# Performance work log

Measured on AMD Instinct MI355X. Metric: run time of the kernel, lower is better.

The kernel has to match this reference:

```python
import jax, jax.numpy as jnp
import numpy as np

CONV_K = 4
C_EXP = 8.0  # Griffin exponent constant
EPS = 1.1920929e-07  # torch RMSNorm default eps = finfo(float32).eps


def rmsnorm(x, w):
    return x * jax.lax.rsqrt(jnp.mean(x * x, axis=-1, keepdims=True) + EPS) * w


def gelu(x):
    return jax.nn.gelu(x, approximate=False)  # torch F.gelu default (erf)


def setup_inputs() -> dict:
    B, T, D = 16, 1024, 1024
    H = 4 * D  # GatedMLP hidden
    key = jax.random.key(0)
    ks = jax.random.split(key, 16)
    s = 0.02
    return {
        "x_seq": jax.random.normal(ks[0], (B, T, D), jnp.float32),
        "h0": jnp.zeros((B, D), jnp.float32),
        "conv_buf": jax.random.normal(ks[1], (B, CONV_K - 1, D), jnp.float32),
        "norm1_w": jnp.ones((D,), jnp.float32),
        "W1": jax.random.normal(ks[2], (D, D), jnp.float32) * s,
        "conv_w": jax.random.normal(ks[3], (D, CONV_K), jnp.float32) * s,
        "conv_b": jnp.zeros((D,), jnp.float32),
        "Wa": jax.random.normal(ks[4], (D, D), jnp.float32) * s,
        "ba": jnp.zeros((D,), jnp.float32),
        "Wx": jax.random.normal(ks[5], (D, D), jnp.float32) * s,
        "bx": jnp.zeros((D,), jnp.float32),
        "log_lambda": jnp.linspace(0.0, 4.0, D).astype(jnp.float32),
        "W2": jax.random.normal(ks[6], (D, D), jnp.float32) * s,
        "Wout": jax.random.normal(ks[7], (D, D), jnp.float32) * s,
        "norm2_w": jnp.ones((D,), jnp.float32),
        "Wg": jax.random.normal(ks[8], (H, D), jnp.float32) * s,
        "Wu": jax.random.normal(ks[9], (H, D), jnp.float32) * s,
        "Wo": jax.random.normal(ks[10], (D, H), jnp.float32) * s,
    }


def _block(x_seq, h0, conv_buf, norm1_w, W1, conv_w, conv_b, Wa, ba, Wx, bx,
           log_lambda, W2, Wout, norm2_w, Wg, Wu, Wo):
    B, T, D = x_seq.shape
    normed = rmsnorm(x_seq, norm1_w)
    b1 = normed @ W1.T                                   # (B,T,D)
    padded = jnp.concatenate([conv_buf, b1], axis=1)     # (B,T+3,D)
    # depthwise causal conv (cross-correlation, matching torch Conv1d)
    b1_conv = conv_b
    for k in range(CONV_K):
        b1_conv = b1_conv + padded[:, k:k + T, :] * conv_w[:, k]
    new_conv_buf = padded[:, -(CONV_K - 1):, :]

    # RG-LRU: precompute gates, scan only the diagonal linear recurrence
    r = jax.nn.sigmoid(b1_conv @ Wa.T + ba)
    i = jax.nn.sigmoid(b1_conv @ Wx.T + bx)
    a = jnp.exp((C_EXP * r) * jax.nn.log_sigmoid(log_lambda))  # sigmoid(L)**(c*r)
    gate = jnp.sqrt(jnp.clip((1.0 - a) * (1.0 + a), 1e-06))
    u = gate * (i * b1_conv)

    def step(h, au):
        a_t, u_t = au
        h = a_t * h + u_t
        return h, h

    new_h, outs = jax.lax.scan(step, h0,
                               (jnp.swapaxes(a, 0, 1), jnp.swapaxes(u, 0, 1)))
    b1_out = jnp.swapaxes(outs, 0, 1)                    # (B,T,D)

    b2 = gelu(normed @ W2.T)
    recurrent_out = (b1_out * b2) @ Wout.T
    x1 = x_seq + recurrent_out

    n2 = rmsnorm(x1, norm2_w)
    mlp = (gelu(n2 @ Wg.T) * (n2 @ Wu.T)) @ Wo.T         # GeGLU gated MLP
    x2 = x1 + mlp
    return x2, new_h, new_conv_buf


def reference(x_seq, h0, conv_buf, norm1_w, W1, conv_w, conv_b, Wa, ba, Wx, bx,
              log_lambda, W2, Wout, norm2_w, Wg, Wu, Wo):
    return _block(x_seq, h0, conv_buf, norm1_w, W1, conv_w, conv_b, Wa, ba,
                  Wx, bx, log_lambda, W2, Wout, norm2_w, Wg, Wu, Wo)
```

## Files before the change

### kernel.cpp

```cpp
#include <hip/hip_runtime.h>
#include <hip/hip_bf16.h>
#include <cstdint>

using bf16 = __hip_bfloat16;
typedef __attribute__((ext_vector_type(8))) short bf16x8;
typedef __attribute__((ext_vector_type(4))) float f32x4;

#define NB 16
#define NT_ 1024
#define ND 1024
#define NH 4096
#define NM (NB * NT_)

enum { EPI_BF16 = 0, EPI_OM, EPI_U, EPI_GELU, EPI_GELU_MUL, EPI_X1, EPI_X2 };

__device__ __forceinline__ float sigm(float x) { return 1.0f / (1.0f + expf(-x)); }
__device__ __forceinline__ float gelu_f(float x) { return 0.5f * x * (1.0f + erff(x * 0.7071067811865476f)); }
__device__ __forceinline__ float b2f(bf16 h) { return __bfloat162float(h); }
__device__ __forceinline__ bf16  f2b(float x) { return __float2bfloat16(x); }

__device__ __forceinline__ void gl_lds16(const bf16* g, void* l) {
  __builtin_amdgcn_global_load_lds((const __attribute__((address_space(1))) void*)g,
                                   (__attribute__((address_space(3))) void*)l, 16, 0, 0);
}

template <int EPI>
__global__ __launch_bounds__(512, 2)
void gemm256(const bf16* __restrict__ A, const bf16* __restrict__ Bw,
             int M, int N, int K,
             const float* __restrict__ biasf, const float* __restrict__ vecf,
             const bf16* __restrict__ auxb, const bf16* __restrict__ auxb2,
             const float* __restrict__ auxf,
             float* __restrict__ outf, bf16* __restrict__ outb)
{
  (void)M;
  __shared__ __align__(16) bf16x8 lds8[8192];
  const int tid  = (int)threadIdx.x;
  const int wave = tid >> 6, lane = tid & 63;
  const int lr = lane & 15, lq = lane >> 4;
  const int wm = wave >> 2, wn = wave & 3;

  const int nwg = (int)gridDim.x;
  const int swz = ((int)blockIdx.x & 7) * (nwg >> 3) + ((int)blockIdx.x >> 3);
  const int nbx = N >> 8;
  const int by = swz / nbx, bx = swz - by * nbx;
  const int m0 = by << 8, n0 = bx << 8;
  const int NT = K >> 6;

  const bf16* __restrict__ Ag = A  + (long)m0 * K;
  const bf16* __restrict__ Bg = Bw + (long)n0 * K;

  const int lrow = lane >> 2;
  const int kbs  = (lane & 3) ^ (((lane >> 5) & 1) << 1);
  const int lqs = lq ^ ((lr & 8) >> 2);
  const int aRd = wm * 512 + lr * 4 + lqs;
  const int bRd = 2048 + wn * 256 + lr * 4 + lqs;

  const bf16 *gA0, *gA1, *gA2, *gA3, *gB0, *gB1, *gB2, *gB3;
  int dA0, dA1, dA2, dA3;
  {
    const int cc0 = wave * 2, cc1 = wave * 2 + 1;
    const int kh0 = cc0 >> 3, kh1 = cc1 >> 3;
    const int r00 = (cc0 & 7) << 4, r01 = (cc1 & 7) << 4;
    const int kc0 = kh0 * 32 + kbs * 8, kc1 = kh1 * 32 + kbs * 8;
    gA0 = Ag + (long)(r00 + lrow) * K + kc0;
    gA1 = Ag + (long)(r01 + lrow) * K + kc1;
    gA2 = Ag + (long)(128 + r00 + lrow) * K + kc0;
    gA3 = Ag + (long)(128 + r01 + lrow) * K + kc1;
    gB0 = Bg + (long)(r00 + lrow) * K + kc0;
    gB1 = Bg + (long)(r01 + lrow) * K + kc1;
    gB2 = Bg + (long)(128 + r00 + lrow) * K + kc0;
    gB3 = Bg + (long)(128 + r01 + lrow) * K + kc1;
    dA0 = kh0 * 16384 + (r00      ) * 64 + lane * 16;
    dA1 = kh1 * 16384 + (r01      ) * 64 + lane * 16;
    dA2 = kh0 * 16384 + (128 + r00) * 64 + lane * 16;
    dA3 = kh1 * 16384 + (128 + r01) * 64 + lane * 16;
  }

#define STAGE_ALL(BUFOFF) do { \
    char* Lb_ = ((char*)lds8) + (BUFOFF); \
    gl_lds16(gA0, Lb_ + dA0);          gl_lds16(gA1, Lb_ + dA1); \
    gl_lds16(gA2, Lb_ + dA2);          gl_lds16(gA3, Lb_ + dA3); \
    gl_lds16(gB0, Lb_ + 32768 + dA0);  gl_lds16(gB1, Lb_ + 32768 + dA1); \
    gl_lds16(gB2, Lb_ + 32768 + dA2);  gl_lds16(gB3, Lb_ + 32768 + dA3); \
    gA0 += 64; gA1 += 64; gA2 += 64; gA3 += 64; \
    gB0 += 64; gB1 += 64; gB2 += 64; gB3 += 64; } while (0)

  f32x4 acc[8][4];
#pragma unroll
  for (int i = 0; i < 8; ++i)
#pragma unroll
    for (int jj = 0; jj < 4; ++jj)
#pragma unroll
      for (int r = 0; r < 4; ++r) acc[i][jj][r] = 0.0f;

  STAGE_ALL(0);
  __syncthreads();

#define TILE2(T, CUR) do { \
    if ((T) + 1 < NT) STAGE_ALL(((CUR) ^ 1) * 65536); \
    const int cb_ = (CUR) * 4096; \
    bf16x8 bF[4][2]; \
    _Pragma("unroll") for (int j_ = 0; j_ < 4; ++j_) { \
      bF[j_][0] = lds8[cb_ + bRd + j_ * 64]; \
      bF[j_][1] = lds8[cb_ + 1024 + bRd + j_ * 64]; } \
    _Pragma("unroll") for (int i_ = 0; i_ < 8; ++i_) { \
      bf16x8 a0_ = lds8[cb_ + aRd + i_ * 64]; \
      bf16x8 a1_ = lds8[cb_ + 1024 + aRd + i_ * 64]; \
      _Pragma("unroll") for (int j_ = 0; j_ < 4; ++j_) { \
        acc[i_][j_] = __builtin_amdgcn_mfma_f32_16x16x32_bf16(a0_, bF[j_][0], acc[i_][j_], 0, 0, 0); \
        acc[i_][j_] = __builtin_amdgcn_mfma_f32_16x16x32_bf16(a1_, bF[j_][1], acc[i_][j_], 0, 0, 0); } } \
    __syncthreads(); \
  } while (0)

  for (int t = 0; t < NT; t += 2) {
    TILE2(t, 0);
    TILE2(t + 1, 1);
  }
#undef TILE2
#undef STAGE_ALL

  const int col0 = n0 + wn * 64 + lr;
  float bj[4], vj[4];
  if constexpr (EPI == EPI_OM || EPI == EPI_U) {
#pragma unroll
    for (int j = 0; j < 4; ++j) bj[j] = biasf[col0 + j * 16];
  }
  if constexpr (EPI == EPI_OM) {
#pragma unroll
    for (int j = 0; j < 4; ++j) vj[j] = -log1pf(expf(-vecf[col0 + j * 16]));
  }
  const long NL = (long)N, N12 = 12 * NL;
  long er = (long)(m0 + wm * 128 + lq * 4) * NL + col0;
#pragma unroll
  for (int i = 0; i < 8; ++i) {
#pragma unroll
    for (int r = 0; r < 4; ++r) {
#pragma unroll
      for (int j = 0; j < 4; ++j) {
        const long idx = er + j * 16;
        float v = acc[i][j][r];
        if constexpr (EPI == EPI_BF16) {
          outb[idx] = f2b(v);
        } else if constexpr (EPI == EPI_OM) {
          float rr = sigm(v + bj[j]);
          outb[idx] = f2b(-expm1f(8.0f * rr * vj[j]));
        } else if constexpr (EPI == EPI_U) {
          float ii = sigm(v + bj[j]);
          float om = b2f(auxb2[idx]);
          float g  = sqrtf(fmaxf(om * (2.0f - om), 1e-6f));
          outb[idx] = f2b(g * ii * b2f(auxb[idx]));
        } else if constexpr (EPI == EPI_GELU) {
          outb[idx] = f2b(gelu_f(v));
        } else if constexpr (EPI == EPI_GELU_MUL) {
          float u2 = b2f(outb[idx]);
          outb[idx] = f2b(gelu_f(v) * u2);
        } else if constexpr (EPI == EPI_X1) {
          outb[idx] = f2b(v + auxf[idx]);
        } else if constexpr (EPI == EPI_X2) {
          outf[idx] = v + b2f(auxb[idx]);
        }
      }
      er += NL;
    }
    er += N12;
  }
}

__global__ __launch_bounds__(256)
void cast4_kernel(const float* __restrict__ in, bf16* __restrict__ out, long n4) {
  long i = (long)blockIdx.x * 256 + threadIdx.x;
  if (i < n4) {
    float4 v = reinterpret_cast<const float4*>(in)[i];
    union { bf16 h[4]; ushort4 u; } pk;
    pk.h[0] = f2b(v.x); pk.h[1] = f2b(v.y); pk.h[2] = f2b(v.z); pk.h[3] = f2b(v.w);
    reinterpret_cast<ushort4*>(out)[i] = pk.u;
  }
}

template <typename TIN>
__global__ __launch_bounds__(256)
void rmsnorm_kernel(const TIN* __restrict__ x, const float* __restrict__ w,
                    bf16* __restrict__ out) {
  const int row = blockIdx.x;
  const int t = threadIdx.x;
  float4 v;
  if constexpr (sizeof(TIN) == 4) {
    v = reinterpret_cast<const float4*>(x + (long)row * ND)[t];
  } else {
    union { ushort4 u; bf16 h[4]; } xv;
    xv.u = reinterpret_cast<const ushort4*>(x + (long)row * ND)[t];
    v = make_float4(b2f(xv.h[0]), b2f(xv.h[1]), b2f(xv.h[2]), b2f(xv.h[3]));
  }
  float ss = v.x * v.x + v.y * v.y + v.z * v.z + v.w * v.w;
#pragma unroll
  for (int off = 32; off > 0; off >>= 1) ss += __shfl_down(ss, off, 64);
  __shared__ float red[4];
  if ((t & 63) == 0) red[t >> 6] = ss;
  __syncthreads();
  float tot = red[0] + red[1] + red[2] + red[3];
  float scale = rsqrtf(tot * (1.0f / ND) + 1.1920929e-07f);
  float4 wv = reinterpret_cast<const float4*>(w)[t];
  union { bf16 h[4]; ushort4 u; } pk;
  pk.h[0] = f2b(v.x * scale * wv.x);
  pk.h[1] = f2b(v.y * scale * wv.y);
  pk.h[2] = f2b(v.z * scale * wv.z);
  pk.h[3] = f2b(v.w * scale * wv.w);
  reinterpret_cast<ushort4*>(out + (long)row * ND)[t] = pk.u;
}

__global__ __launch_bounds__(256)
void conv_kernel(const bf16* __restrict__ b1, const float* __restrict__ conv_buf,
                 const float* __restrict__ conv_w, const float* __restrict__ conv_b,
                 bf16* __restrict__ out_b1c, float* __restrict__ out_newbuf) {
  const long gid = (long)blockIdx.x * 256 + threadIdx.x;
  const int d = (int)(gid & (ND - 1));
  const long bt = gid >> 10;
  const int t = (int)(bt & (NT_ - 1));
  const int b = (int)(bt >> 10);
  float acc = conv_b[d];
#pragma unroll
  for (int k = 0; k < 4; ++k) {
    const int p = t + k;
    float src = (p < 3) ? conv_buf[((long)b * 3 + p) * ND + d]
                        : b2f(b1[((long)b * NT_ + (p - 3)) * ND + d]);
    acc = fmaf(conv_w[d * 4 + k], src, acc);
  }
  out_b1c[gid] = f2b(acc);
  if (t >= NT_ - 3)
    out_newbuf[((long)b * 3 + (t - (NT_ - 3))) * ND + d] = b2f(b1[gid]);
}

__global__ __launch_bounds__(256)
void scan_kernel(const bf16* __restrict__ om, const bf16* __restrict__ u,
                 const bf16* __restrict__ b2, const float* __restrict__ h0,
                 bf16* __restrict__ prod, float* __restrict__ newh) {
  const int gid = blockIdx.x * 256 + threadIdx.x;
  const int d = gid & (ND - 1);
  const int b = gid >> 10;
  float h = h0[gid];
  const long base = (long)b * NT_ * ND + d;
#pragma unroll 8
  for (int t = 0; t < NT_; ++t) {
    const long idx = base + (long)t * ND;
    h = fmaf(-b2f(om[idx]), h, h) + b2f(u[idx]);
    prod[idx] = f2b(h * b2f(b2[idx]));
  }
  newh[gid] = h;
}

extern "C" void kernel_launch(void* const* d_in, const int* in_sizes, int n_in,
                              void* d_out, int out_size, void* d_ws, size_t ws_size,
                              hipStream_t stream) {
  const float* x_seq    = (const float*)d_in[0];
  const float* h0       = (const float*)d_in[1];
  const float* conv_buf = (const float*)d_in[2];
  const float* norm1_w  = (const float*)d_in[3];
  const float* W1       = (const float*)d_in[4];
  const float* conv_w   = (const float*)d_in[5];
  const float* conv_b   = (const float*)d_in[6];
  const float* Wa       = (const float*)d_in[7];
  const float* ba       = (const float*)d_in[8];
  const float* Wx       = (const float*)d_in[9];
  const float* bx       = (const float*)d_in[10];
  const float* loglam   = (const float*)d_in[11];
  const float* W2       = (const float*)d_in[12];
  const float* Wout     = (const float*)d_in[13];
  const float* norm2_w  = (const float*)d_in[14];
  const float* Wg       = (const float*)d_in[15];
  const float* Wu       = (const float*)d_in[16];
  const float* Wo       = (const float*)d_in[17];

  char* ws = (char*)d_ws;
  bf16* normed = (bf16*)(ws);
  bf16* b1buf  = (bf16*)(ws + (32L  << 20));
  bf16* b1cbuf = (bf16*)(ws + (64L  << 20));
  bf16* Woutb  = (bf16*)(ws + (64L  << 20));
  bf16* ombuf  = (bf16*)(ws + (96L  << 20));
  bf16* ubuf   = (bf16*)(ws + (128L << 20));
  bf16* x1buf  = (bf16*)(ws + (160L << 20));
  bf16* b2buf  = x1buf;
  bf16* bigbuf = (bf16*)(ws + (32L  << 20));
  bf16* W1b    = (bf16*)(ws + (192L << 20));
  bf16* Wab    = (bf16*)(ws + (194L << 20));
  bf16* Wxb    = (bf16*)(ws + (196L << 20));
  bf16* W2b    = (bf16*)(ws + (198L << 20));
  bf16* Wgb    = (bf16*)(ws + (200L << 20));
  bf16* Wub    = (bf16*)(ws + (208L << 20));
  bf16* Wob    = (bf16*)(ws + (216L << 20));

  float* out_x2 = (float*)d_out;
  float* out_h  = out_x2 + (long)NM * ND;
  float* out_cb = out_h + NB * ND;

  const dim3 blk(256);
  const dim3 blk512(512);
  const dim3 gD256((NM / 256) * (ND / 256));
  const dim3 gH256((NM / 256) * (NH / 256));

  cast4_kernel<<<dim3(1024), blk, 0, stream>>>(W1, W1b, 262144);
  cast4_kernel<<<dim3(1024), blk, 0, stream>>>(Wa, Wab, 262144);
  cast4_kernel<<<dim3(1024), blk, 0, stream>>>(Wx, Wxb, 262144);
  cast4_kernel<<<dim3(1024), blk, 0, stream>>>(W2, W2b, 262144);
  cast4_kernel<<<dim3(4096), blk, 0, stream>>>(Wg, Wgb, 1048576);
  cast4_kernel<<<dim3(4096), blk, 0, stream>>>(Wu, Wub, 1048576);
  cast4_kernel<<<dim3(4096), blk, 0, stream>>>(Wo, Wob, 1048576);

  rmsnorm_kernel<float><<<dim3(NM), blk, 0, stream>>>(x_seq, norm1_w, normed);
  gemm256<EPI_BF16><<<gD256, blk512, 0, stream>>>(normed, W1b, NM, ND, ND,
      nullptr, nullptr, nullptr, nullptr, nullptr, nullptr, b1buf);
  conv_kernel<<<dim3((NM * ND) / 256), blk, 0, stream>>>(b1buf, conv_buf, conv_w, conv_b,
      b1cbuf, out_cb);
  gemm256<EPI_OM><<<gD256, blk512, 0, stream>>>(b1cbuf, Wab, NM, ND, ND,
      ba, loglam, nullptr, nullptr, nullptr, nullptr, ombuf);
  gemm256<EPI_U><<<gD256, blk512, 0, stream>>>(b1cbuf, Wxb, NM, ND, ND,
      bx, nullptr, b1cbuf, ombuf, nullptr, nullptr, ubuf);
  gemm256<EPI_GELU><<<gD256, blk512, 0, stream>>>(normed, W2b, NM, ND, ND,
      nullptr, nullptr, nullptr, nullptr, nullptr, nullptr, b2buf);
  scan_kernel<<<dim3(NB * ND / 256), blk, 0, stream>>>(ombuf, ubuf, b2buf, h0, b1buf, out_h);
  cast4_kernel<<<dim3(1024), blk, 0, stream>>>(Wout, Woutb, 262144);
  gemm256<EPI_X1><<<gD256, blk512, 0, stream>>>(b1buf, Woutb, NM, ND, ND,
      nullptr, nullptr, nullptr, nullptr, x_seq, nullptr, x1buf);
  rmsnorm_kernel<bf16><<<dim3(NM), blk, 0, stream>>>(x1buf, norm2_w, normed);
  gemm256<EPI_BF16><<<gH256, blk512, 0, stream>>>(normed, Wub, NM, NH, ND,
      nullptr, nullptr, nullptr, nullptr, nullptr, nullptr, bigbuf);
  gemm256<EPI_GELU_MUL><<<gH256, blk512, 0, stream>>>(normed, Wgb, NM, NH, ND,
      nullptr, nullptr, nullptr, nullptr, nullptr, nullptr, bigbuf);
  gemm256<EPI_X2><<<gD256, blk512, 0, stream>>>(bigbuf, Wob, NM, ND, NH,
      nullptr, nullptr, x1buf, nullptr, nullptr, out_x2, nullptr);
}
```

Baseline: 1.141 ms.

## Use a 4-stage ring-buffered K pipeline with BK=32 in the GEMM

The GEMM main loop moves from a double-buffered 64-wide K tile with two __syncthreads per step to four 32-wide K buffers. Loads are prefetched two tiles ahead. Explicit s_waitcnt vmcnt counts plus a single s_barrier per tile replace the full syncs, so global-to-LDS loads overlap with MFMA work for longer and fewer barriers run per K chunk. In exchange, each tile does less MFMA work per barrier. Correctness now depends on hand-counted vmcnt values matching the number of loads each stage issues.

Measured after the change: 1.148 ms. Within noise of the previous version (+0.7%).

```diff
diff --git a/kernel.cpp b/kernel.cpp
--- a/kernel.cpp
+++ b/kernel.cpp
@@ -45,7 +45,7 @@
   const int nbx = N >> 8;
   const int by = swz / nbx, bx = swz - by * nbx;
   const int m0 = by << 8, n0 = bx << 8;
-  const int NT = K >> 6;
+  const int NT = K >> 5;
 
   const bf16* __restrict__ Ag = A  + (long)m0 * K;
   const bf16* __restrict__ Bg = Bw + (long)n0 * K;
@@ -53,38 +53,28 @@
   const int lrow = lane >> 2;
   const int kbs  = (lane & 3) ^ (((lane >> 5) & 1) << 1);
   const int lqs = lq ^ ((lr & 8) >> 2);
-  const int aRd = wm * 512 + lr * 4 + lqs;
-  const int bRd = 2048 + wn * 256 + lr * 4 + lqs;
-
-  const bf16 *gA0, *gA1, *gA2, *gA3, *gB0, *gB1, *gB2, *gB3;
-  int dA0, dA1, dA2, dA3;
+  const int lr4lqs = lr * 4 + lqs;
+  const int aRd = wm * 512 + lr4lqs;
+  const int bRd = 1024 + wn * 256 + lr4lqs;
+
+  const bf16 *gA0, *gA1, *gB0, *gB1;
+  int dA0, dA1;
   {
     const int cc0 = wave * 2, cc1 = wave * 2 + 1;
-    const int kh0 = cc0 >> 3, kh1 = cc1 >> 3;
-    const int r00 = (cc0 & 7) << 4, r01 = (cc1 & 7) << 4;
-    const int kc0 = kh0 * 32 + kbs * 8, kc1 = kh1 * 32 + kbs * 8;
-    gA0 = Ag + (long)(r00 + lrow) * K + kc0;
-    gA1 = Ag + (long)(r01 + lrow) * K + kc1;
-    gA2 = Ag + (long)(128 + r00 + lrow) * K + kc0;
-    gA3 = Ag + (long)(128 + r01 + lrow) * K + kc1;
-    gB0 = Bg + (long)(r00 + lrow) * K + kc0;
-    gB1 = Bg + (long)(r01 + lrow) * K + kc1;
-    gB2 = Bg + (long)(128 + r00 + lrow) * K + kc0;
-    gB3 = Bg + (long)(128 + r01 + lrow) * K + kc1;
-    dA0 = kh0 * 16384 + (r00      ) * 64 + lane * 16;
-    dA1 = kh1 * 16384 + (r01      ) * 64 + lane * 16;
-    dA2 = kh0 * 16384 + (128 + r00) * 64 + lane * 16;
-    dA3 = kh1 * 16384 + (128 + r01) * 64 + lane * 16;
-  }
-
-#define STAGE_ALL(BUFOFF) do { \
-    char* Lb_ = ((char*)lds8) + (BUFOFF); \
+    const int kc = kbs * 8;
+    gA0 = Ag + (long)(cc0 * 16 + lrow) * K + kc;
+    gA1 = Ag + (long)(cc1 * 16 + lrow) * K + kc;
+    gB0 = Bg + (long)(cc0 * 16 + lrow) * K + kc;
+    gB1 = Bg + (long)(cc1 * 16 + lrow) * K + kc;
+    dA0 = cc0 * 1024 + lane * 16;
+    dA1 = cc1 * 1024 + lane * 16;
+  }
+
+#define STAGE(BUFIDX) do { \
+    char* Lb_ = ((char*)lds8) + (BUFIDX) * 32768; \
     gl_lds16(gA0, Lb_ + dA0);          gl_lds16(gA1, Lb_ + dA1); \
-    gl_lds16(gA2, Lb_ + dA2);          gl_lds16(gA3, Lb_ + dA3); \
-    gl_lds16(gB0, Lb_ + 32768 + dA0);  gl_lds16(gB1, Lb_ + 32768 + dA1); \
-    gl_lds16(gB2, Lb_ + 32768 + dA2);  gl_lds16(gB3, Lb_ + 32768 + dA3); \
-    gA0 += 64; gA1 += 64; gA2 += 64; gA3 += 64; \
-    gB0 += 64; gB1 += 64; gB2 += 64; gB3 += 64; } while (0)
+    gl_lds16(gB0, Lb_ + 16384 + dA0);  gl_lds16(gB1, Lb_ + 16384 + dA1); \
+    gA0 += 32; gA1 += 32; gB0 += 32; gB1 += 32; } while (0)
 
   f32x4 acc[8][4];
 #pragma unroll
@@ -94,31 +84,38 @@
 #pragma unroll
       for (int r = 0; r < 4; ++r) acc[i][jj][r] = 0.0f;
 
-  STAGE_ALL(0);
-  __syncthreads();
-
-#define TILE2(T, CUR) do { \
-    if ((T) + 1 < NT) STAGE_ALL(((CUR) ^ 1) * 65536); \
-    const int cb_ = (CUR) * 4096; \
-    bf16x8 bF[4][2]; \
-    _Pragma("unroll") for (int j_ = 0; j_ < 4; ++j_) { \
-      bF[j_][0] = lds8[cb_ + bRd + j_ * 64]; \
-      bF[j_][1] = lds8[cb_ + 1024 + bRd + j_ * 64]; } \
+  STAGE(0);
+  STAGE(1);
+
+#define KTILE(T, BUF) do { \
+    if ((T) + 2 < NT) { \
+      STAGE(((BUF) + 2) & 3); \
+      asm volatile("s_waitcnt vmcnt(8)" ::: "memory"); \
+    } else if ((T) + 1 < NT) { \
+      asm volatile("s_waitcnt vmcnt(4)" ::: "memory"); \
+    } else { \
+      asm volatile("s_waitcnt vmcnt(0)" ::: "memory"); \
+    } \
+    asm volatile("s_barrier" ::: "memory"); \
+    const int cb_ = (BUF) * 2048; \
+    bf16x8 bF[4]; \
+    _Pragma("unroll") for (int j_ = 0; j_ < 4; ++j_) \
+      bF[j_] = lds8[cb_ + bRd + j_ * 64]; \
     _Pragma("unroll") for (int i_ = 0; i_ < 8; ++i_) { \
-      bf16x8 a0_ = lds8[cb_ + aRd + i_ * 64]; \
-      bf16x8 a1_ = lds8[cb_ + 1024 + aRd + i_ * 64]; \
-      _Pragma("unroll") for (int j_ = 0; j_ < 4; ++j_) { \
-        acc[i_][j_] = __builtin_amdgcn_mfma_f32_16x16x32_bf16(a0_, bF[j_][0], acc[i_][j_], 0, 0, 0); \
-        acc[i_][j_] = __builtin_amdgcn_mfma_f32_16x16x32_bf16(a1_, bF[j_][1], acc[i_][j_], 0, 0, 0); } } \
-    __syncthreads(); \
+      bf16x8 a_ = lds8[cb_ + aRd + i_ * 64]; \
+      _Pragma("unroll") for (int j_ = 0; j_ < 4; ++j_) \
+        acc[i_][j_] = __builtin_amdgcn_mfma_f32_16x16x32_bf16(a_, bF[j_], acc[i_][j_], 0, 0, 0); \
+    } \
   } while (0)
 
-  for (int t = 0; t < NT; t += 2) {
-    TILE2(t, 0);
-    TILE2(t + 1, 1);
-  }
-#undef TILE2
-#undef STAGE_ALL
+  for (int t = 0; t < NT; t += 4) {
+    KTILE(t + 0, 0);
+    KTILE(t + 1, 1);
+    KTILE(t + 2, 2);
+    KTILE(t + 3, 3);
+  }
+#undef KTILE
+#undef STAGE
 
   const int col0 = n0 + wn * 64 + lr;
   float bj[4], vj[4];
```
